# Performance work log

Hardware: AMD Instinct MI355X
Metric: run time of the kernel (lower is better)

The kernel has to match this reference:

```python
import jax, jax.numpy as jnp
import numpy as np

N = 50000   # nodes (WSI patches)
G = 8       # graphs in batch
E = 400000  # edges (k-NN patch graph)
D = 512     # in_channels
HC = 512    # hidden_channels (fixed by Linear(512,*) in pooling)
OUT = 1     # out_channels (binary, sigmoid+squeeze)


def segment_softmax(e, idx, num_segments):
    m = jax.ops.segment_max(e, idx, num_segments=num_segments)
    m = jnp.where(jnp.isfinite(m), m, 0.0)
    ex = jnp.exp(e - m[idx])
    s = jax.ops.segment_sum(ex, idx, num_segments=num_segments)
    return ex / (s[idx] + 1e-16)


def setup_inputs() -> dict:
    key = jax.random.key(0)
    ks = jax.random.split(key, 16)
    x = jax.random.normal(ks[0], (N, D), jnp.float32)
    src = jax.random.randint(ks[1], (E,), 0, N)
    dst = jax.random.randint(ks[2], (E,), 0, N)
    edge_index = jnp.stack([src, dst]).astype(jnp.int64)
    batch = jnp.sort(jax.random.randint(ks[3], (N,), 0, G)).astype(jnp.int64)
    sc = 1.0 / np.sqrt(D).astype(np.float32)
    return {
        "x": x,
        "edge_index": edge_index,
        "batch": batch,
        # GATConv (heads=1, concat=True defaults)
        "W": jax.random.normal(ks[4], (D, HC), jnp.float32) * sc,
        "att_src": jax.random.normal(ks[5], (HC,), jnp.float32) * sc,
        "att_dst": jax.random.normal(ks[6], (HC,), jnp.float32) * sc,
        "b_conv": jnp.zeros((HC,), jnp.float32),
        # AttentionalAggregation: gate_nn = Linear(512,1), nn = Linear(512,512)
        "Wg": jax.random.normal(ks[7], (HC, 1), jnp.float32) * sc,
        "bg": jnp.zeros((1,), jnp.float32),
        "Wn": jax.random.normal(ks[8], (HC, HC), jnp.float32) * sc,
        "bn": jnp.zeros((HC,), jnp.float32),
        # classifier head
        "W1": jax.random.normal(ks[9], (HC, HC), jnp.float32) * sc,
        "b1": jnp.zeros((HC,), jnp.float32),
        "W2": jax.random.normal(ks[10], (HC, OUT), jnp.float32) * sc,
        "b2": jnp.zeros((OUT,), jnp.float32),
    }


def reference(x, edge_index, batch, W, att_src, att_dst, b_conv,
              Wg, bg, Wn, bn, W1, b1, W2, b2):
    # ---- GATConv (heads=1): linear, per-edge attention, segment softmax ----
    h = x @ W  # [N, HC]
    loops = jnp.arange(N, dtype=edge_index.dtype)
    src = jnp.concatenate([edge_index[0], loops])  # add_self_loops=True
    dst = jnp.concatenate([edge_index[1], loops])
    a_s = h @ att_src  # [N]
    a_d = h @ att_dst  # [N]
    e = jax.nn.leaky_relu(a_s[src] + a_d[dst], 0.2)     # [E+N]
    alpha = segment_softmax(e, dst, N)                  # softmax over incoming edges
    hconv = jax.ops.segment_sum(alpha[:, None] * h[src], dst, num_segments=N)
    hconv = hconv + b_conv  # [N, HC]
    # (Dropout omitted: deterministic eval reference)

    # ---- AttentionalAggregation over batch index ----
    gate = hconv @ Wg + bg                 # [N, 1]
    xn = hconv @ Wn + bn                   # [N, HC]
    g = segment_softmax(gate[:, 0], batch, G)[:, None]  # [N, 1]
    pooled = jax.ops.segment_sum(g * xn, batch, num_segments=G)  # [G, HC]

    # ---- classifier head ----
    out = jax.nn.relu(pooled @ W1 + b1)
    out = jnp.squeeze(jax.nn.sigmoid(out @ W2 + b2))  # [G]
    return out, g
```

## Files before the change

kernel.cpp:

```cpp
#include <hip/hip_runtime.h>
#include <stdint.h>

#define N_NODES 50000
#define N_PAD   50048
#define GQ      8
#define EE      400000
#define DIM     512
#define CAPE    128
#define NBLK_SCAN 196
#define EDGE_BLOCKS 1024

typedef __attribute__((ext_vector_type(8))) __bf16 bf16x8;
typedef __attribute__((ext_vector_type(4))) float f32x4;
typedef __attribute__((ext_vector_type(2))) float f32x2;

__device__ __forceinline__ unsigned short f2bf(float f){
  unsigned u = __float_as_uint(f);
  return (unsigned short)((u + 0x7fffu + ((u >> 16) & 1u)) >> 16);
}
__device__ __forceinline__ unsigned pk2(float lo, float hi){
  return (unsigned)f2bf(lo) | ((unsigned)f2bf(hi) << 16);
}
__device__ __forceinline__ float dot4(float4 a, float4 b){ return a.x*b.x + a.y*b.y + a.z*b.z + a.w*b.w; }
__device__ __forceinline__ float wredSum(float v){
#pragma unroll
  for (int o = 32; o > 0; o >>= 1) v += __shfl_xor(v, o, 64);
  return v;
}
__device__ __forceinline__ float rlanef(float v, int l){
  return __int_as_float(__builtin_amdgcn_readlane(__float_as_int(v), l));
}
__device__ __forceinline__ void gload_lds16(const void* g, void* l){
  __builtin_amdgcn_global_load_lds((__attribute__((address_space(1))) void*)g,
                                   (__attribute__((address_space(3))) void*)l, 16, 0, 0);
}
__device__ __forceinline__ unsigned char f2fp8(float x){
  return (unsigned char)__builtin_amdgcn_cvt_pk_fp8_f32(x, x, 0, false);
}
__device__ __forceinline__ unsigned pk4f8(float a, float b, float c, float d){
  unsigned w = (unsigned)__builtin_amdgcn_cvt_pk_fp8_f32(a, b, 0, false);
  return (unsigned)__builtin_amdgcn_cvt_pk_fp8_f32(c, d, (int)w, true);
}
__device__ __forceinline__ void consumeF8(f32x2* ac, uint2 u, float al){
  f32x2 p0 = __builtin_amdgcn_cvt_pk_f32_fp8(u.x, false);
  f32x2 p1 = __builtin_amdgcn_cvt_pk_f32_fp8(u.x, true);
  f32x2 p2 = __builtin_amdgcn_cvt_pk_f32_fp8(u.y, false);
  f32x2 p3 = __builtin_amdgcn_cvt_pk_f32_fp8(u.y, true);
  ac[0] += al * p0;
  ac[1] += al * p1;
  ac[2] += al * p2;
  ac[3] += al * p3;
}

static constexpr size_t AL(size_t x){ return (x + 255) & ~(size_t)255; }
static constexpr size_t OFF_XBF   = 0;
static constexpr size_t OFF_HF8   = OFF_XBF   + AL((size_t)N_PAD * DIM * 2);
static constexpr size_t OFF_HCV8  = OFF_HF8   + AL((size_t)N_PAD * DIM);
static constexpr size_t OFF_CAP   = OFF_HCV8  + AL((size_t)N_NODES * DIM);
static constexpr size_t OFF_WTBF  = OFF_CAP   + AL((size_t)N_NODES * CAPE * 8);
static constexpr size_t OFF_WNT   = OFF_WTBF  + AL((size_t)DIM * DIM * 2);
static constexpr size_t OFF_W1T   = OFF_WNT   + AL((size_t)DIM * DIM * 4);
static constexpr size_t OFF_WSS   = OFF_W1T   + AL((size_t)DIM * DIM * 4);
static constexpr size_t OFF_WSD   = OFF_WSS   + AL((size_t)DIM * 4);
static constexpr size_t OFF_AS    = OFF_WSD   + AL((size_t)DIM * 4);
static constexpr size_t OFF_AD    = OFF_AS    + AL((size_t)N_NODES * 4);
static constexpr size_t OFF_GATE  = OFF_AD    + AL((size_t)N_NODES * 4);
static constexpr size_t OFF_CNT   = OFF_GATE  + AL((size_t)N_NODES * 4);
static constexpr size_t OFF_GSUM  = OFF_CNT   + AL((size_t)N_NODES * 4);
static constexpr size_t OFF_PP    = OFF_GSUM  + AL((size_t)GQ * 4);
static constexpr size_t OFF_POOL  = OFF_PP    + AL((size_t)GQ * DIM * 4);
static constexpr size_t OFF_Z1    = OFF_POOL  + AL((size_t)GQ * DIM * 4);


__global__ void k_setup(const float* __restrict__ W, const float* __restrict__ atS,
                        const float* __restrict__ atD, const float* __restrict__ Wn,
                        const float* __restrict__ W1,
                        float* ws_s, float* ws_d,
                        unsigned short* __restrict__ WtBf, float* __restrict__ WnT,
                        float* __restrict__ W1T,
                        int* cnt, float* gsum, float* pp){
  __shared__ float tile[64][65];
  int bx = blockIdx.x;
  if (bx < NBLK_SCAN){
    int i = bx * 256 + threadIdx.x;
    if (i < N_NODES) cnt[i] = 1;
    if (i < GQ) gsum[i] = 0.f;
    if (i < GQ * DIM) pp[i] = 0.f;
    if (bx < 128){
      int wid = threadIdx.x >> 6, lane = threadIdx.x & 63;
      int k = bx * 4 + wid;
      const float4* row = (const float4*)(W + (size_t)k * DIM);
      float4 r0 = row[lane * 2], r1 = row[lane * 2 + 1];
      const float4* s4 = (const float4*)atS;
      const float4* d4 = (const float4*)atD;
      float vs = dot4(r0, s4[lane * 2]) + dot4(r1, s4[lane * 2 + 1]);
      float vd = dot4(r0, d4[lane * 2]) + dot4(r1, d4[lane * 2 + 1]);
      vs = wredSum(vs); vd = wredSum(vd);
      if (lane == 0){ ws_s[k] = vs; ws_d[k] = vd; }
    }
  } else {
    int tb = bx - NBLK_SCAN;
    int y = tb >> 6, bq = tb & 63;
    const float* src = (y == 0) ? W : (y == 1) ? Wn : W1;
    int bi = bq & 7, bj = bq >> 3;
    int r0 = bi * 64, c0 = bj * 64;
#pragma unroll
    for (int ii = 0; ii < 16; ++ii){
      int idx = ii * 256 + threadIdx.x;
      int r = idx >> 6, c = idx & 63;
      tile[r][c] = src[(size_t)(r0 + r) * DIM + c0 + c];
    }
    __syncthreads();
#pragma unroll
    for (int ii = 0; ii < 16; ++ii){
      int idx = ii * 256 + threadIdx.x;
      int cc = idx >> 6, rr = idx & 63;
      float v = tile[rr][cc];
      size_t o = (size_t)(c0 + cc) * DIM + r0 + rr;
      if (y == 0) WtBf[o] = f2bf(v);
      else if (y == 1) WnT[o] = v;
      else W1T[o] = v;
    }
  }
}

__global__ __launch_bounds__(256) void k_cast(const float* __restrict__ x,
                                              const float* __restrict__ ws_s,
                                              const float* __restrict__ ws_d,
                                              unsigned short* __restrict__ x_bf,
                                              float* __restrict__ a_s, float* __restrict__ a_d,
                                              int2* __restrict__ cap){
  int wid = threadIdx.x >> 6, lane = threadIdx.x & 63;
  size_t i = (size_t)blockIdx.x * 4 + wid;
  if (i >= N_PAD) return;
  unsigned short* orow = x_bf + i * DIM;
  if (i >= N_NODES){
    ((uint4*)orow)[lane] = make_uint4(0, 0, 0, 0);
    return;
  }
  const float4* xr = (const float4*)(x + i * DIM);
  float4 v0 = xr[lane * 2], v1 = xr[lane * 2 + 1];
  ((uint4*)orow)[lane] = make_uint4(pk2(v0.x, v0.y), pk2(v0.z, v0.w), pk2(v1.x, v1.y), pk2(v1.z, v1.w));
  const float4* s4 = (const float4*)ws_s;
  const float4* d4 = (const float4*)ws_d;
  float vs = dot4(v0, s4[lane * 2]) + dot4(v1, s4[lane * 2 + 1]);
  float vd = dot4(v0, d4[lane * 2]) + dot4(v1, d4[lane * 2 + 1]);
  vs = wredSum(vs); vd = wredSum(vd);
  if (lane == 0){
    a_s[i] = vs; a_d[i] = vd;
    cap[i * CAPE] = make_int2((int)(i << 9), __float_as_int(vs));
  }
}

__global__ void k_fill(const int* __restrict__ ei, const float* __restrict__ a_s,
                       int* cnt, int2* __restrict__ cap){
  int e = blockIdx.x * 256 + threadIdx.x;
  if (e < EE){
    int s = ei[e], d = ei[EE + e];
    int p = atomicAdd(&cnt[d], 1);
    if (p < CAPE) cap[(size_t)d * CAPE + p] = make_int2(s << 9, __float_as_int(a_s[s]));
  }
}

__global__ __launch_bounds__(256, 2) void k_gemm(const unsigned short* __restrict__ A,
                                                 const unsigned short* __restrict__ Bt,
                                                 unsigned char* __restrict__ H8){
  __shared__ unsigned short As[128 * 32];
  __shared__ unsigned short Bs[256 * 32];
  const int tid = threadIdx.x;
  const int wid = tid >> 6, lane = tid & 63, quad = lane >> 4, l16 = lane & 15;
  const int m0 = blockIdx.x * 128, n0 = blockIdx.y * 256;
  const int wm = (wid & 1) * 64, wn = (wid >> 1) * 128;
  const int qa = quad ^ ((l16 >> 1) & 3);
  f32x4 acc[4][8] = {};
  for (int kt = 0; kt < 16; ++kt){
    const int k0 = kt * 32;
    __syncthreads();
#pragma unroll
    for (int r = 0; r < 2; ++r){
      int p = r * 256 + tid;
      int mm = p >> 2;
      int qg = (p & 3) ^ ((mm >> 1) & 3);
      gload_lds16(A + (size_t)(m0 + mm) * DIM + k0 + qg * 8,
                  As + (size_t)(r * 256 + wid * 64) * 8);
    }
#pragma unroll
    for (int r = 0; r < 4; ++r){
      int p = r * 256 + tid;
      int mm = p >> 2;
      int qg = (p & 3) ^ ((mm >> 1) & 3);
      gload_lds16(Bt + (size_t)(n0 + mm) * DIM + k0 + qg * 8,
                  Bs + (size_t)(r * 256 + wid * 64) * 8);
    }
    __syncthreads();
    bf16x8 af[4], bfr[8];
#pragma unroll
    for (int f = 0; f < 4; ++f)
      af[f]  = *(const bf16x8*)(As + (wm + f * 16 + l16) * 32 + qa * 8);
#pragma unroll
    for (int f = 0; f < 8; ++f)
      bfr[f] = *(const bf16x8*)(Bs + (wn + f * 16 + l16) * 32 + qa * 8);
#pragma unroll
    for (int fm = 0; fm < 4; ++fm)
#pragma unroll
      for (int fn = 0; fn < 8; ++fn)
        acc[fm][fn] = __builtin_amdgcn_mfma_f32_16x16x32_bf16(af[fm], bfr[fn], acc[fm][fn], 0, 0, 0);
  }
#pragma unroll
  for (int fm = 0; fm < 4; ++fm){
#pragma unroll
    for (int r = 0; r < 4; ++r){
      size_t gro = (size_t)(m0 + wm + fm * 16 + quad * 4 + r) * DIM + n0 + wn + l16;
#pragma unroll
      for (int fn = 0; fn < 8; ++fn)
        H8[gro + fn * 16] = f2fp8(acc[fm][fn][r]);
    }
  }
}

__global__ __launch_bounds__(256, 8) void k_edge(const int* __restrict__ cnt, const int2* __restrict__ cap,
                                              const float* __restrict__ a_d,
                                              const unsigned char* __restrict__ h8,
                                              const float* __restrict__ bconv,
                                              const float* __restrict__ Wg, const float* __restrict__ bg,
                                              unsigned char* __restrict__ hconv8, float* __restrict__ gate){
  int wid = threadIdx.x >> 6, lane = threadIdx.x & 63;
  for (int i = blockIdx.x * 4 + wid; i < N_NODES; i += EDGE_BLOCKS * 4){
    int deg = cnt[i]; if (deg > CAPE) deg = CAPE;
    const int2* row = cap + (size_t)i * CAPE;
    float adi = a_d[i];
    f32x2 ac[4] = {};

    if (deg <= 64){
      int off_l = 0;
      float x0 = 0.f;
      if (lane < deg){
        int2 c = row[lane]; off_l = c.x;
        float e = __int_as_float(c.y) + adi; e = (e > 0.f) ? e : 0.2f * e;
        x0 = __expf(e);
      }
      float inv = 1.f / (wredSum(x0) + 1e-16f);
      float x0n = x0 * inv;
      int degc = (deg + 3) & ~3;

      auto FETCH = [&](int jj, uint2& u, float& al){
        int off = __builtin_amdgcn_readlane(off_l, jj);
        al = rlanef(x0n, jj);
        u = *((const uint2*)(h8 + off) + lane);
      };
      uint2 u0, u1, u2, u3;
      float f0, f1, f2, f3;
      FETCH(0, u0, f0); FETCH(1, u1, f1); FETCH(2, u2, f2); FETCH(3, u3, f3);
      for (int j = 0; j < degc; j += 4){
        consumeF8(ac, u0, f0); if (j + 4 < degc) FETCH(j + 4, u0, f0);
        consumeF8(ac, u1, f1); if (j + 5 < degc) FETCH(j + 5, u1, f1);
        consumeF8(ac, u2, f2); if (j + 6 < degc) FETCH(j + 6, u2, f2);
        consumeF8(ac, u3, f3); if (j + 7 < degc) FETCH(j + 7, u3, f3);
      }
    } else {
      int o0 = 0, o1 = 0;
      float x0 = 0.f, x1 = 0.f;
      {
        int2 c = row[lane]; o0 = c.x;
        float e = __int_as_float(c.y) + adi; e = (e > 0.f) ? e : 0.2f * e;
        x0 = __expf(e);
      }
      if (64 + lane < deg){
        int2 c = row[64 + lane]; o1 = c.x;
        float e = __int_as_float(c.y) + adi; e = (e > 0.f) ? e : 0.2f * e;
        x1 = __expf(e);
      }
      float inv = 1.f / (wredSum(x0 + x1) + 1e-16f);
      float xn0 = x0 * inv, xn1 = x1 * inv;
      for (int j = 0; j < deg; ++j){
        int off  = __builtin_amdgcn_readlane((j < 64) ? o0 : o1, j & 63);
        float al = rlanef((j < 64) ? xn0 : xn1, j & 63);
        uint2 u = *((const uint2*)(h8 + off) + lane);
        consumeF8(ac, u, al);
      }
    }

    float4 bc0 = ((const float4*)bconv)[lane * 2];
    float4 bc1 = ((const float4*)bconv)[lane * 2 + 1];
    ac[0][0] += bc0.x; ac[0][1] += bc0.y; ac[1][0] += bc0.z; ac[1][1] += bc0.w;
    ac[2][0] += bc1.x; ac[2][1] += bc1.y; ac[3][0] += bc1.z; ac[3][1] += bc1.w;
    unsigned w0 = pk4f8(ac[0][0], ac[0][1], ac[1][0], ac[1][1]);
    unsigned w1 = pk4f8(ac[2][0], ac[2][1], ac[3][0], ac[3][1]);
    ((uint2*)(hconv8 + (size_t)i * DIM))[lane] = make_uint2(w0, w1);
    float4 wg0 = ((const float4*)Wg)[lane * 2];
    float4 wg1 = ((const float4*)Wg)[lane * 2 + 1];
    float gp = ac[0][0]*wg0.x + ac[0][1]*wg0.y + ac[1][0]*wg0.z + ac[1][1]*wg0.w
             + ac[2][0]*wg1.x + ac[2][1]*wg1.y + ac[3][0]*wg1.z + ac[3][1]*wg1.w;
    gp = wredSum(gp);
    if (lane == 0) gate[i] = gp + bg[0];
  }
}

__global__ void k_gsum(const float* __restrict__ gate, const int* __restrict__ batch, float* gsum){
  __shared__ float sm[GQ];
  int t = threadIdx.x, i = blockIdx.x * 512 + t;
  if (t < GQ) sm[t] = 0.f;
  __syncthreads();
  if (i < N_NODES) atomicAdd(&sm[batch[i]], __expf(gate[i]));
  __syncthreads();
  if (t < GQ && sm[t] != 0.f) atomicAdd(&gsum[t], sm[t]);
}

__global__ __launch_bounds__(256) void k_pool(const unsigned char* __restrict__ hconv8,
                                              const int* __restrict__ batch,
                                              const float* __restrict__ gate,
                                              const float* __restrict__ gsum,
                                              float* __restrict__ out_g, float* pp){
  __shared__ float gv_s[128];
  __shared__ int b_s[128];
  int t = threadIdx.x;
  int base = blockIdx.x * 128;
  if (t < 128){
    int i = base + t;
    if (i < N_NODES){
      int b = batch[i];
      float gv = __expf(gate[i]) / (gsum[b] + 1e-16f);
      gv_s[t] = gv; b_s[t] = b;
      out_g[i] = gv;
    } else { gv_s[t] = 0.f; b_s[t] = -1; }
  }
  __syncthreads();
  int lim = N_NODES - base; if (lim > 128) lim = 128;
  float ax = 0.f, ay = 0.f;
  int cur = b_s[0];
#pragma unroll 4
  for (int r = 0; r < lim; ++r){
    int b = b_s[r];
    float gv = gv_s[r];
    if (b != cur){
      atomicAdd(&pp[cur * DIM + 2 * t], ax);
      atomicAdd(&pp[cur * DIM + 2 * t + 1], ay);
      ax = ay = 0.f; cur = b;
    }
    unsigned us = *(const unsigned short*)(hconv8 + (size_t)(base + r) * DIM + 2 * t);
    auto p = __builtin_amdgcn_cvt_pk_f32_fp8(us, false);
    ax += gv * p[0];
    ay += gv * p[1];
  }
  if (cur >= 0){
    atomicAdd(&pp[cur * DIM + 2 * t], ax);
    atomicAdd(&pp[cur * DIM + 2 * t + 1], ay);
  }
}

template<bool RELU>
__global__ void k_headA(const float* __restrict__ src, const float* __restrict__ WT,
                        const float* __restrict__ bias, float* dst){
  __shared__ float sp[GQ * DIM];
  int t = threadIdx.x;
  for (int idx = t; idx < GQ * DIM; idx += 256) sp[idx] = src[idx];
  __syncthreads();
  int wid = t >> 6, lane = t & 63;
  int j = blockIdx.x * 4 + wid;
  const float4* wr = (const float4*)(WT + (size_t)j * DIM);
  float4 w0 = wr[lane * 2], w1 = wr[lane * 2 + 1];
  float bj = bias[j];
#pragma unroll
  for (int g = 0; g < GQ; ++g){
    const float* pg = sp + g * DIM + lane * 8;
    float s = w0.x*pg[0] + w0.y*pg[1] + w0.z*pg[2] + w0.w*pg[3]
            + w1.x*pg[4] + w1.y*pg[5] + w1.z*pg[6] + w1.w*pg[7];
    s = wredSum(s);
    if (lane == 0){
      s += bj;
      if (RELU) s = fmaxf(s, 0.f);
      dst[g * DIM + j] = s;
    }
  }
}

__global__ void k_headC(const float* __restrict__ z1, const float* __restrict__ W2,
                        const float* __restrict__ b2, float* __restrict__ out){
  int wv = threadIdx.x >> 6, lane = threadIdx.x & 63;
  const float4* zr = (const float4*)(z1 + (size_t)wv * DIM);
  const float4* w4 = (const float4*)W2;
  float s = dot4(zr[lane * 2], w4[lane * 2]) + dot4(zr[lane * 2 + 1], w4[lane * 2 + 1]);
  s = wredSum(s);
  if (lane == 0) out[wv] = 1.f / (1.f + __expf(-(s + b2[0])));
}

extern "C" void kernel_launch(void* const* d_in, const int* in_sizes, int n_in,
                              void* d_out, int out_size, void* d_ws, size_t ws_size,
                              hipStream_t stream){
  (void)in_sizes; (void)n_in; (void)out_size; (void)ws_size;
  const float* x   = (const float*)d_in[0];
  const int*   ei  = (const int*)d_in[1];
  const int*   bat = (const int*)d_in[2];
  const float* W   = (const float*)d_in[3];
  const float* atS = (const float*)d_in[4];
  const float* atD = (const float*)d_in[5];
  const float* bcv = (const float*)d_in[6];
  const float* Wg  = (const float*)d_in[7];
  const float* bg  = (const float*)d_in[8];
  const float* Wn  = (const float*)d_in[9];
  const float* bn  = (const float*)d_in[10];
  const float* W1  = (const float*)d_in[11];
  const float* b1  = (const float*)d_in[12];
  const float* W2  = (const float*)d_in[13];
  const float* b2  = (const float*)d_in[14];
  float* out = (float*)d_out;
  char* ws = (char*)d_ws;

  unsigned short* x_bf   = (unsigned short*)(ws + OFF_XBF);
  unsigned char*  h8     = (unsigned char*)(ws + OFF_HF8);
  unsigned char*  hconv8 = (unsigned char*)(ws + OFF_HCV8);
  int2*           cap    = (int2*)(ws + OFF_CAP);
  unsigned short* Wt_bf  = (unsigned short*)(ws + OFF_WTBF);
  float* WnT  = (float*)(ws + OFF_WNT);
  float* W1T  = (float*)(ws + OFF_W1T);
  float* ws_s = (float*)(ws + OFF_WSS);
  float* ws_d = (float*)(ws + OFF_WSD);
  float* a_s  = (float*)(ws + OFF_AS);
  float* a_d  = (float*)(ws + OFF_AD);
  float* gate = (float*)(ws + OFF_GATE);
  int* cnt  = (int*)(ws + OFF_CNT);
  float* gsum = (float*)(ws + OFF_GSUM);
  float* pp   = (float*)(ws + OFF_PP);
  float* pool = (float*)(ws + OFF_POOL);
  float* z1   = (float*)(ws + OFF_Z1);

  hipLaunchKernelGGL(k_setup, dim3(NBLK_SCAN + 192), dim3(256), 0, stream,
                     W, atS, atD, Wn, W1, ws_s, ws_d, Wt_bf, WnT, W1T, cnt, gsum, pp);
  hipLaunchKernelGGL(k_cast, dim3(N_PAD / 4), dim3(256), 0, stream,
                     x, ws_s, ws_d, x_bf, a_s, a_d, cap);
  hipLaunchKernelGGL(k_fill, dim3((EE + 255) / 256), dim3(256), 0, stream, ei, a_s, cnt, cap);
  hipLaunchKernelGGL(k_gemm, dim3(N_PAD / 128, 2), dim3(256), 0, stream, x_bf, Wt_bf, h8);
  hipLaunchKernelGGL(k_edge, dim3(EDGE_BLOCKS), dim3(256), 0, stream,
                     cnt, cap, a_d, h8, bcv, Wg, bg, hconv8, gate);
  hipLaunchKernelGGL(k_gsum, dim3(98), dim3(512), 0, stream, gate, bat, gsum);
  hipLaunchKernelGGL(k_pool, dim3((N_NODES + 127) / 128), dim3(256), 0, stream,
                     hconv8, bat, gate, gsum, out + GQ, pp);
  hipLaunchKernelGGL((k_headA<false>), dim3(128), dim3(256), 0, stream, pp, WnT, bn, pool);
  hipLaunchKernelGGL((k_headA<true>),  dim3(128), dim3(256), 0, stream, pool, W1T, b1, z1);
  hipLaunchKernelGGL(k_headC, dim3(1), dim3(512), 0, stream, z1, W2, b2, out);
}
```

Measured before the change: 368.5 us.

## Double-buffer GEMM LDS tiles and grid-stride the cast kernel

The bf16 GEMM now keeps two LDS buffers and issues global-to-LDS loads for the next K tile before running MFMAs on the current one, with one barrier per iteration instead of two. This aims to hide global load latency behind compute, at the cost of doubled LDS (48KB per block), which may reduce occupancy. Separately, the cast kernel changes from one block per four rows to a fixed 2048-block grid-stride loop, cutting block launch overhead. The single barrier after compute relies on the async LDS loads having completed, so correctness depends on the load/wait semantics of gload_lds16.

```diff
diff --git a/kernel.cpp b/kernel.cpp
--- a/kernel.cpp
+++ b/kernel.cpp
@@ -9,6 +9,7 @@
 #define CAPE    128
 #define NBLK_SCAN 196
 #define EDGE_BLOCKS 1024
+#define CAST_BLOCKS 2048
 
 typedef __attribute__((ext_vector_type(8))) __bf16 bf16x8;
 typedef __attribute__((ext_vector_type(4))) float f32x4;
@@ -131,24 +132,24 @@
                                               float* __restrict__ a_s, float* __restrict__ a_d,
                                               int2* __restrict__ cap){
   int wid = threadIdx.x >> 6, lane = threadIdx.x & 63;
-  size_t i = (size_t)blockIdx.x * 4 + wid;
-  if (i >= N_PAD) return;
-  unsigned short* orow = x_bf + i * DIM;
-  if (i >= N_NODES){
-    ((uint4*)orow)[lane] = make_uint4(0, 0, 0, 0);
-    return;
-  }
-  const float4* xr = (const float4*)(x + i * DIM);
-  float4 v0 = xr[lane * 2], v1 = xr[lane * 2 + 1];
-  ((uint4*)orow)[lane] = make_uint4(pk2(v0.x, v0.y), pk2(v0.z, v0.w), pk2(v1.x, v1.y), pk2(v1.z, v1.w));
   const float4* s4 = (const float4*)ws_s;
   const float4* d4 = (const float4*)ws_d;
-  float vs = dot4(v0, s4[lane * 2]) + dot4(v1, s4[lane * 2 + 1]);
-  float vd = dot4(v0, d4[lane * 2]) + dot4(v1, d4[lane * 2 + 1]);
-  vs = wredSum(vs); vd = wredSum(vd);
-  if (lane == 0){
-    a_s[i] = vs; a_d[i] = vd;
-    cap[i * CAPE] = make_int2((int)(i << 9), __float_as_int(vs));
+  for (int i = blockIdx.x * 4 + wid; i < N_PAD; i += CAST_BLOCKS * 4){
+    unsigned short* orow = x_bf + (size_t)i * DIM;
+    if (i >= N_NODES){
+      ((uint4*)orow)[lane] = make_uint4(0, 0, 0, 0);
+      continue;
+    }
+    const float4* xr = (const float4*)(x + (size_t)i * DIM);
+    float4 v0 = xr[lane * 2], v1 = xr[lane * 2 + 1];
+    ((uint4*)orow)[lane] = make_uint4(pk2(v0.x, v0.y), pk2(v0.z, v0.w), pk2(v1.x, v1.y), pk2(v1.z, v1.w));
+    float vs = dot4(v0, s4[lane * 2]) + dot4(v1, s4[lane * 2 + 1]);
+    float vd = dot4(v0, d4[lane * 2]) + dot4(v1, d4[lane * 2 + 1]);
+    vs = wredSum(vs); vd = wredSum(vd);
+    if (lane == 0){
+      a_s[i] = vs; a_d[i] = vd;
+      cap[(size_t)i * CAPE] = make_int2((int)(i << 9), __float_as_int(vs));
+    }
   }
 }
 
@@ -165,24 +166,23 @@
 __global__ __launch_bounds__(256, 2) void k_gemm(const unsigned short* __restrict__ A,
                                                  const unsigned short* __restrict__ Bt,
                                                  unsigned char* __restrict__ H8){
-  __shared__ unsigned short As[128 * 32];
-  __shared__ unsigned short Bs[256 * 32];
+  __shared__ unsigned short As[2][128 * 32];
+  __shared__ unsigned short Bs[2][256 * 32];
   const int tid = threadIdx.x;
   const int wid = tid >> 6, lane = tid & 63, quad = lane >> 4, l16 = lane & 15;
   const int m0 = blockIdx.x * 128, n0 = blockIdx.y * 256;
   const int wm = (wid & 1) * 64, wn = (wid >> 1) * 128;
   const int qa = quad ^ ((l16 >> 1) & 3);
-  f32x4 acc[4][8] = {};
-  for (int kt = 0; kt < 16; ++kt){
+
+  auto STAGE = [&](int b, int kt){
     const int k0 = kt * 32;
-    __syncthreads();
 #pragma unroll
     for (int r = 0; r < 2; ++r){
       int p = r * 256 + tid;
       int mm = p >> 2;
       int qg = (p & 3) ^ ((mm >> 1) & 3);
       gload_lds16(A + (size_t)(m0 + mm) * DIM + k0 + qg * 8,
-                  As + (size_t)(r * 256 + wid * 64) * 8);
+                  As[b] + (size_t)(r * 256 + wid * 64) * 8);
     }
 #pragma unroll
     for (int r = 0; r < 4; ++r){
@@ -190,21 +190,30 @@
       int mm = p >> 2;
       int qg = (p & 3) ^ ((mm >> 1) & 3);
       gload_lds16(Bt + (size_t)(n0 + mm) * DIM + k0 + qg * 8,
-                  Bs + (size_t)(r * 256 + wid * 64) * 8);
-    }
-    __syncthreads();
+                  Bs[b] + (size_t)(r * 256 + wid * 64) * 8);
+    }
+  };
+
+  f32x4 acc[4][8] = {};
+  STAGE(0, 0);
+  __syncthreads();
+  int cur = 0;
+  for (int kt = 0; kt < 16; ++kt){
+    if (kt + 1 < 16) STAGE(cur ^ 1, kt + 1);
     bf16x8 af[4], bfr[8];
 #pragma unroll
     for (int f = 0; f < 4; ++f)
-      af[f]  = *(const bf16x8*)(As + (wm + f * 16 + l16) * 32 + qa * 8);
+      af[f]  = *(const bf16x8*)(As[cur] + (wm + f * 16 + l16) * 32 + qa * 8);
 #pragma unroll
     for (int f = 0; f < 8; ++f)
-      bfr[f] = *(const bf16x8*)(Bs + (wn + f * 16 + l16) * 32 + qa * 8);
+      bfr[f] = *(const bf16x8*)(Bs[cur] + (wn + f * 16 + l16) * 32 + qa * 8);
 #pragma unroll
     for (int fm = 0; fm < 4; ++fm)
 #pragma unroll
       for (int fn = 0; fn < 8; ++fn)
         acc[fm][fn] = __builtin_amdgcn_mfma_f32_16x16x32_bf16(af[fm], bfr[fn], acc[fm][fn], 0, 0, 0);
+    __syncthreads();
+    cur ^= 1;
   }
 #pragma unroll
   for (int fm = 0; fm < 4; ++fm){
@@ -426,7 +435,7 @@
 
   hipLaunchKernelGGL(k_setup, dim3(NBLK_SCAN + 192), dim3(256), 0, stream,
                      W, atS, atD, Wn, W1, ws_s, ws_d, Wt_bf, WnT, W1T, cnt, gsum, pp);
-  hipLaunchKernelGGL(k_cast, dim3(N_PAD / 4), dim3(256), 0, stream,
+  hipLaunchKernelGGL(k_cast, dim3(CAST_BLOCKS), dim3(256), 0, stream,
                      x, ws_s, ws_d, x_bf, a_s, a_d, cap);
   hipLaunchKernelGGL(k_fill, dim3((EE + 255) / 256), dim3(256), 0, stream, ei, a_s, cnt, cap);
   hipLaunchKernelGGL(k_gemm, dim3(N_PAD / 128, 2), dim3(256), 0, stream, x_bf, Wt_bf, h8);
```

Result: no change. 373.6 us (+1.4%).

## Split edge aggregation into two column-half passes for better cache locality

Applied to the files above, without the earlier changes.

The edge gather kernel now runs twice, each pass covering 256 of the 512 fp8 feature columns. Each lane loads 4 bytes per neighbour instead of 8. The intent is to halve the gathered working set of h8 per pass so it fits better in the L2/MALL cache and random gathers hit more often. The cost is redoing the edge softmax and index reads twice, plus a second launch, and the gate value is now accumulated across the two passes with a read-modify-write.

```diff
diff --git a/kernel.cpp b/kernel.cpp
--- a/kernel.cpp
+++ b/kernel.cpp
@@ -41,15 +41,11 @@
   unsigned w = (unsigned)__builtin_amdgcn_cvt_pk_fp8_f32(a, b, 0, false);
   return (unsigned)__builtin_amdgcn_cvt_pk_fp8_f32(c, d, (int)w, true);
 }
-__device__ __forceinline__ void consumeF8(f32x2* ac, uint2 u, float al){
-  f32x2 p0 = __builtin_amdgcn_cvt_pk_f32_fp8(u.x, false);
-  f32x2 p1 = __builtin_amdgcn_cvt_pk_f32_fp8(u.x, true);
-  f32x2 p2 = __builtin_amdgcn_cvt_pk_f32_fp8(u.y, false);
-  f32x2 p3 = __builtin_amdgcn_cvt_pk_f32_fp8(u.y, true);
+__device__ __forceinline__ void consume4(f32x2* ac, unsigned u, float al){
+  f32x2 p0 = __builtin_amdgcn_cvt_pk_f32_fp8(u, false);
+  f32x2 p1 = __builtin_amdgcn_cvt_pk_f32_fp8(u, true);
   ac[0] += al * p0;
   ac[1] += al * p1;
-  ac[2] += al * p2;
-  ac[3] += al * p3;
 }
 
 static constexpr size_t AL(size_t x){ return (x + 255) & ~(size_t)255; }
@@ -223,13 +219,14 @@
                                               const unsigned char* __restrict__ h8,
                                               const float* __restrict__ bconv,
                                               const float* __restrict__ Wg, const float* __restrict__ bg,
-                                              unsigned char* __restrict__ hconv8, float* __restrict__ gate){
+                                              unsigned char* __restrict__ hconv8, float* __restrict__ gate,
+                                              int colofs, int pass){
   int wid = threadIdx.x >> 6, lane = threadIdx.x & 63;
   for (int i = blockIdx.x * 4 + wid; i < N_NODES; i += EDGE_BLOCKS * 4){
     int deg = cnt[i]; if (deg > CAPE) deg = CAPE;
     const int2* row = cap + (size_t)i * CAPE;
     float adi = a_d[i];
-    f32x2 ac[4] = {};
+    f32x2 ac[2] = {};
 
     if (deg <= 64){
       int off_l = 0;
@@ -243,19 +240,19 @@
       float x0n = x0 * inv;
       int degc = (deg + 3) & ~3;
 
-      auto FETCH = [&](int jj, uint2& u, float& al){
+      auto FETCH = [&](int jj, unsigned& u, float& al){
         int off = __builtin_amdgcn_readlane(off_l, jj);
         al = rlanef(x0n, jj);
-        u = *((const uint2*)(h8 + off) + lane);
+        u = *((const unsigned*)(h8 + off + colofs) + lane);
       };
-      uint2 u0, u1, u2, u3;
+      unsigned u0, u1, u2, u3;
       float f0, f1, f2, f3;
       FETCH(0, u0, f0); FETCH(1, u1, f1); FETCH(2, u2, f2); FETCH(3, u3, f3);
       for (int j = 0; j < degc; j += 4){
-        consumeF8(ac, u0, f0); if (j + 4 < degc) FETCH(j + 4, u0, f0);
-        consumeF8(ac, u1, f1); if (j + 5 < degc) FETCH(j + 5, u1, f1);
-        consumeF8(ac, u2, f2); if (j + 6 < degc) FETCH(j + 6, u2, f2);
-        consumeF8(ac, u3, f3); if (j + 7 < degc) FETCH(j + 7, u3, f3);
+        consume4(ac, u0, f0); if (j + 4 < degc) FETCH(j + 4, u0, f0);
+        consume4(ac, u1, f1); if (j + 5 < degc) FETCH(j + 5, u1, f1);
+        consume4(ac, u2, f2); if (j + 6 < degc) FETCH(j + 6, u2, f2);
+        consume4(ac, u3, f3); if (j + 7 < degc) FETCH(j + 7, u3, f3);
       }
     } else {
       int o0 = 0, o1 = 0;
@@ -275,24 +272,22 @@
       for (int j = 0; j < deg; ++j){
         int off  = __builtin_amdgcn_readlane((j < 64) ? o0 : o1, j & 63);
         float al = rlanef((j < 64) ? xn0 : xn1, j & 63);
-        uint2 u = *((const uint2*)(h8 + off) + lane);
-        consumeF8(ac, u, al);
+        unsigned u = *((const unsigned*)(h8 + off + colofs) + lane);
+        consume4(ac, u, al);
       }
     }
 
-    float4 bc0 = ((const float4*)bconv)[lane * 2];
-    float4 bc1 = ((const float4*)bconv)[lane * 2 + 1];
-    ac[0][0] += bc0.x; ac[0][1] += bc0.y; ac[1][0] += bc0.z; ac[1][1] += bc0.w;
-    ac[2][0] += bc1.x; ac[2][1] += bc1.y; ac[3][0] += bc1.z; ac[3][1] += bc1.w;
-    unsigned w0 = pk4f8(ac[0][0], ac[0][1], ac[1][0], ac[1][1]);
-    unsigned w1 = pk4f8(ac[2][0], ac[2][1], ac[3][0], ac[3][1]);
-    ((uint2*)(hconv8 + (size_t)i * DIM))[lane] = make_uint2(w0, w1);
-    float4 wg0 = ((const float4*)Wg)[lane * 2];
-    float4 wg1 = ((const float4*)Wg)[lane * 2 + 1];
-    float gp = ac[0][0]*wg0.x + ac[0][1]*wg0.y + ac[1][0]*wg0.z + ac[1][1]*wg0.w
-             + ac[2][0]*wg1.x + ac[2][1]*wg1.y + ac[3][0]*wg1.z + ac[3][1]*wg1.w;
+    float4 bc = ((const float4*)(bconv + colofs))[lane];
+    ac[0][0] += bc.x; ac[0][1] += bc.y; ac[1][0] += bc.z; ac[1][1] += bc.w;
+    unsigned w = pk4f8(ac[0][0], ac[0][1], ac[1][0], ac[1][1]);
+    ((unsigned*)(hconv8 + (size_t)i * DIM + colofs))[lane] = w;
+    float4 wg = ((const float4*)(Wg + colofs))[lane];
+    float gp = ac[0][0]*wg.x + ac[0][1]*wg.y + ac[1][0]*wg.z + ac[1][1]*wg.w;
     gp = wredSum(gp);
-    if (lane == 0) gate[i] = gp + bg[0];
+    if (lane == 0){
+      if (pass == 0) gate[i] = gp;
+      else           gate[i] = gate[i] + gp + bg[0];
+    }
   }
 }
 
@@ -431,7 +426,9 @@
   hipLaunchKernelGGL(k_fill, dim3((EE + 255) / 256), dim3(256), 0, stream, ei, a_s, cnt, cap);
   hipLaunchKernelGGL(k_gemm, dim3(N_PAD / 128, 2), dim3(256), 0, stream, x_bf, Wt_bf, h8);
   hipLaunchKernelGGL(k_edge, dim3(EDGE_BLOCKS), dim3(256), 0, stream,
-                     cnt, cap, a_d, h8, bcv, Wg, bg, hconv8, gate);
+                     cnt, cap, a_d, h8, bcv, Wg, bg, hconv8, gate, 0, 0);
+  hipLaunchKernelGGL(k_edge, dim3(EDGE_BLOCKS), dim3(256), 0, stream,
+                     cnt, cap, a_d, h8, bcv, Wg, bg, hconv8, gate, 256, 1);
   hipLaunchKernelGGL(k_gsum, dim3(98), dim3(512), 0, stream, gate, bat, gsum);
   hipLaunchKernelGGL(k_pool, dim3((N_NODES + 127) / 128), dim3(256), 0, stream,
                      hconv8, bat, gate, gsum, out + GQ, pp);
```

New measurement: 398.3 us. +8.1%, slower.
